# Kernel optimization log

Hardware: AMD Instinct MI355X
Metric: run time of the kernel (lower is better)

The kernel has to match this reference:

```python
import jax, jax.numpy as jnp
import numpy as np

B, N, C, D, H, L, F = 64, 256, 16, 512, 8, 8, 2048
HD = D // H
PI = np.pi


def _ln(x, w, b, eps=1e-5):
    mu = jnp.mean(x, -1, keepdims=True)
    var = jnp.mean(jnp.square(x - mu), -1, keepdims=True)
    return (x - mu) * jax.lax.rsqrt(var + eps) * w + b


def _forward(x_node, x_full, Wp, bp, cls, e_w1, e_b1, e_w2, e_b2, edge_scale,
             qkv_w, qkv_b, out_w, out_b, ln1_w, ln1_b, ln2_w, ln2_b,
             ff1_w, ff1_b, ff2_w, ff2_b, cl_ln_w, cl_ln_b, cl_w1, cl_b1, cl_w2, cl_b2):
    Bq, Nq, _ = x_node.shape
    # pairwise kaon geometry from absolute y/phi
    y = x_full[:, :, 14]
    phi = x_full[:, :, 15]
    dy = jnp.abs(y[:, :, None] - y[:, None, :])                                  # [B,N,N]
    dphi = jnp.abs(jnp.mod(phi[:, :, None] - phi[:, None, :] + PI, 2 * PI) - PI)
    dr = jnp.sqrt(dy * dy + dphi * dphi + 1e-8)
    ef = jnp.stack([dy, dphi, dr], -1)                                           # [B,N,N,3]
    hmid = jax.nn.gelu(ef @ e_w1.T + e_b1, approximate=False)                    # [B,N,N,16]
    raw = hmid @ e_w2.T + e_b2                                                   # [B,N,N,H]
    central = jnp.mean(raw, axis=2).transpose(0, 2, 1)                           # [B,H,N]
    edge_bias = raw.transpose(0, 3, 1, 2)                                        # [B,H,N,N]
    bias = jnp.zeros((Bq, H, Nq + 1, Nq + 1), x_node.dtype)
    bias = bias.at[:, :, 1:, 1:].set(edge_bias)
    bias = bias.at[:, :, 0, 1:].set(central * edge_scale)
    bias = bias.at[:, :, 1:, 0].set(central * edge_scale)

    h = x_node @ Wp.T + bp
    h = jnp.concatenate([jnp.broadcast_to(cls, (Bq, 1, D)), h], axis=1)          # [B,S,D]
    S = Nq + 1
    scale = 1.0 / np.sqrt(HD)
    for l in range(L):  # pre-norm TransformerEncoderLayer (activation=relu, no final norm)
        x = _ln(h, ln1_w[l], ln1_b[l])
        qkv = x @ qkv_w[l].T + qkv_b[l]
        q, k, v = jnp.split(qkv, 3, axis=-1)
        q = q.reshape(Bq, S, H, HD).transpose(0, 2, 1, 3)
        k = k.reshape(Bq, S, H, HD).transpose(0, 2, 1, 3)
        v = v.reshape(Bq, S, H, HD).transpose(0, 2, 1, 3)
        scores = jnp.einsum('bhqd,bhkd->bhqk', q, k) * scale + bias
        attn = jax.nn.softmax(scores, axis=-1)
        o = jnp.einsum('bhqk,bhkd->bhqd', attn, v).transpose(0, 2, 1, 3).reshape(Bq, S, D)
        h = h + o @ out_w[l].T + out_b[l]
        x = _ln(h, ln2_w[l], ln2_b[l])
        h = h + jax.nn.relu(x @ ff1_w[l].T + ff1_b[l]) @ ff2_w[l].T + ff2_b[l]
    x = _ln(h[:, 0], cl_ln_w, cl_ln_b)
    return jax.nn.gelu(x @ cl_w1.T + cl_b1, approximate=False) @ cl_w2.T + cl_b2  # [B,2]


def setup_inputs() -> dict:
    key = jax.random.key(0)
    ks = iter(jax.random.split(key, 40))
    f32 = jnp.float32

    def nrm(shape, s=0.02):
        return (s * jax.random.normal(next(ks), shape)).astype(f32)

    return {
        'x_node': jax.random.normal(next(ks), (B, N, C), f32),
        'x_full': jax.random.normal(next(ks), (B, N, 16), f32),
        'Wp': nrm((D, C)), 'bp': jnp.zeros((D,), f32),
        'cls': nrm((1, 1, D)),
        'e_w1': nrm((16, 3), 0.3), 'e_b1': jnp.zeros((16,), f32),
        'e_w2': nrm((H, 16), 0.01), 'e_b2': jnp.zeros((H,), f32),
        'edge_scale': jnp.full((1,), 0.1, f32),
        'qkv_w': nrm((L, 3 * D, D)), 'qkv_b': jnp.zeros((L, 3 * D), f32),
        'out_w': nrm((L, D, D)), 'out_b': jnp.zeros((L, D), f32),
        'ln1_w': jnp.ones((L, D), f32), 'ln1_b': jnp.zeros((L, D), f32),
        'ln2_w': jnp.ones((L, D), f32), 'ln2_b': jnp.zeros((L, D), f32),
        'ff1_w': nrm((L, F, D)), 'ff1_b': jnp.zeros((L, F), f32),
        'ff2_w': nrm((L, D, F)), 'ff2_b': jnp.zeros((L, D), f32),
        'cl_ln_w': jnp.ones((D,), f32), 'cl_ln_b': jnp.zeros((D,), f32),
        'cl_w1': nrm((D // 2, D)), 'cl_b1': jnp.zeros((D // 2,), f32),
        'cl_w2': nrm((2, D // 2)), 'cl_b2': jnp.zeros((2,), f32),
    }


def reference(x_node, x_full, Wp, bp, cls, e_w1, e_b1, e_w2, e_b2, edge_scale,
              qkv_w, qkv_b, out_w, out_b, ln1_w, ln1_b, ln2_w, ln2_b,
              ff1_w, ff1_b, ff2_w, ff2_b, cl_ln_w, cl_ln_b, cl_w1, cl_b1, cl_w2, cl_b2):
    return _forward(x_node, x_full, Wp, bp, cls, e_w1, e_b1, e_w2, e_b2, edge_scale,
                    qkv_w, qkv_b, out_w, out_b, ln1_w, ln1_b, ln2_w, ln2_b,
                    ff1_w, ff1_b, ff2_w, ff2_b, cl_ln_w, cl_ln_b, cl_w1, cl_b1, cl_w2, cl_b2)
```

## Files before the change

### kernel.cpp

```cpp
#include <hip/hip_runtime.h>
#include <hip/hip_bf16.h>
#include <stdint.h>

#define PI_F     3.14159265358979323846f
#define TWO_PI_F 6.28318530717958647692f

typedef __attribute__((ext_vector_type(8))) short bf16x8;
typedef __attribute__((ext_vector_type(4))) float f32x4;

#define BB 64
#define NN 256
#define SS 257
#define DD 512
#define HH 8
#define HDD 64
#define LL 8
#define MTOK 16448
#define MPAD 16512
#define BSTR 264
#define VSTR 320

__device__ __forceinline__ float b2f(unsigned short u){
  union { float f; uint32_t i; } c; c.i = ((uint32_t)u) << 16; return c.f;
}
__device__ __forceinline__ unsigned short f2b(float f){
  union { float f; uint32_t i; } c; c.f = f;
  uint32_t r = c.i + 0x7FFFu + ((c.i >> 16) & 1u);
  return (unsigned short)(r >> 16);
}

typedef __attribute__((address_space(1))) unsigned char ga_t;
typedef __attribute__((address_space(3))) unsigned char ls_t;
__device__ __forceinline__ void gl_lds16(const void* g, void* l){
  __builtin_amdgcn_global_load_lds((ga_t*)g, (ls_t*)l, 16, 0, 0);
}

__global__ __launch_bounds__(256) void cvt_kernel(const float* __restrict__ src,
                                                  unsigned short* __restrict__ dst, int n2){
  int i = blockIdx.x*256 + threadIdx.x;
  int stride = gridDim.x*256;
  for (; i < n2; i += stride){
    float2 v = ((const float2*)src)[i];
    ((uint32_t*)dst)[i] = (uint32_t)f2b(v.x) | ((uint32_t)f2b(v.y) << 16);
  }
}

__global__ __launch_bounds__(256) void edge_kernel(
    const float* __restrict__ x_full, const float* __restrict__ e_w1, const float* __restrict__ e_b1,
    const float* __restrict__ e_w2, const float* __restrict__ e_b2,
    unsigned short* __restrict__ bias, float* __restrict__ central)
{
  const int bi = blockIdx.x;
  const int b = bi >> 8, i = bi & 255;
  const int j = threadIdx.x;
  const float yi = x_full[((long)b*NN + i)*16 + 14];
  const float fi = x_full[((long)b*NN + i)*16 + 15];
  const float yj = x_full[((long)b*NN + j)*16 + 14];
  const float fj = x_full[((long)b*NN + j)*16 + 15];
  const float dy = fabsf(yi - yj);
  float md = fmodf(fi - fj + PI_F, TWO_PI_F);
  if (md < 0.f) md += TWO_PI_F;
  const float dphi = fabsf(md - PI_F);
  const float dr = sqrtf(dy*dy + dphi*dphi + 1e-8f);
  float raw[8];
  #pragma unroll
  for (int hh = 0; hh < 8; ++hh) raw[hh] = e_b2[hh];
  #pragma unroll
  for (int k = 0; k < 16; ++k){
    float z = e_w1[k*3]*dy + e_w1[k*3+1]*dphi + e_w1[k*3+2]*dr + e_b1[k];
    float g = 0.5f*z*(1.f + erff(z*0.70710678118f));
    #pragma unroll
    for (int hh = 0; hh < 8; ++hh) raw[hh] += g * e_w2[hh*16 + k];
  }
  #pragma unroll
  for (int hh = 0; hh < 8; ++hh)
    bias[(((long)b*HH + hh)*SS + 1 + i)*BSTR + 1 + j] = f2b(raw[hh]);
  #pragma unroll
  for (int m = 1; m < 64; m <<= 1)
    #pragma unroll
    for (int hh = 0; hh < 8; ++hh) raw[hh] += __shfl_xor(raw[hh], m);
  __shared__ float cw[4][8];
  const int wv = j >> 6;
  if ((j & 63) == 0)
    for (int hh = 0; hh < 8; ++hh) cw[wv][hh] = raw[hh];
  __syncthreads();
  if (j < 8){
    float t = cw[0][j] + cw[1][j] + cw[2][j] + cw[3][j];
    central[((long)b*NN + i)*HH + j] = t * (1.f/NN);
  }
}

__global__ __launch_bounds__(256) void edge_border_kernel(
    const float* __restrict__ central, const float* __restrict__ edge_scale,
    unsigned short* __restrict__ bias)
{
  const int bh = blockIdx.x;
  const int b = bh >> 3, h = bh & 7;
  const int j = threadIdx.x;
  const float es = edge_scale[0];
  const float cv = central[((long)b*NN + j)*HH + h] * es;
  const long base = (long)bh*SS*BSTR;
  const unsigned short u = f2b(cv);
  bias[base + 1 + j] = u;
  bias[base + (long)(1+j)*BSTR] = u;
  if (j == 0) bias[base] = 0;
}

__global__ __launch_bounds__(256) void proj_kernel(
    const float* __restrict__ x_node, const float* __restrict__ Wp,
    const float* __restrict__ bp, const float* __restrict__ cls, float* __restrict__ hb)
{
  const int t = blockIdx.x;
  const int tid = threadIdx.x;
  const int b = t / SS, s2 = t - b*SS;
  float2 o;
  if (s2 == 0){
    o = *(const float2*)(cls + tid*2);
  } else {
    const float* xr = x_node + ((long)b*NN + (s2-1))*16;
    float xv[16];
    #pragma unroll
    for (int c2 = 0; c2 < 16; ++c2) xv[c2] = xr[c2];
    float oo[2];
    #pragma unroll
    for (int e = 0; e < 2; ++e){
      int d = tid*2 + e;
      float a = bp[d];
      const float* wr2 = Wp + (long)d*16;
      #pragma unroll
      for (int c2 = 0; c2 < 16; ++c2) a += xv[c2]*wr2[c2];
      oo[e] = a;
    }
    o.x = oo[0]; o.y = oo[1];
  }
  *(float2*)(hb + (long)t*DD + tid*2) = o;
}

__global__ __launch_bounds__(256) void ln_kernel(
    const float* __restrict__ hb, const float* __restrict__ w,
    const float* __restrict__ bbv, unsigned short* __restrict__ xb)
{
  const int t = blockIdx.x;
  const int tid = threadIdx.x;
  const float2 v = *(const float2*)(hb + (long)t*DD + tid*2);
  float s = v.x + v.y;
  float ss = v.x*v.x + v.y*v.y;
  #pragma unroll
  for (int m = 1; m < 64; m <<= 1){ s += __shfl_xor(s, m); ss += __shfl_xor(ss, m); }
  __shared__ float red[8];
  const int wv = tid >> 6;
  if ((tid & 63) == 0){ red[wv] = s; red[4+wv] = ss; }
  __syncthreads();
  s  = red[0]+red[1]+red[2]+red[3];
  ss = red[4]+red[5]+red[6]+red[7];
  const float mu = s * (1.f/DD);
  const float var = ss * (1.f/DD) - mu*mu;
  const float rs = rsqrtf(var + 1e-5f);
  const float2 wv2 = *(const float2*)(w + tid*2);
  const float2 bv2 = *(const float2*)(bbv + tid*2);
  float o0 = (v.x - mu)*rs*wv2.x + bv2.x;
  float o1 = (v.y - mu)*rs*wv2.y + bv2.y;
  ((uint32_t*)xb)[(long)t*256 + tid] = (uint32_t)f2b(o0) | ((uint32_t)f2b(o1) << 16);
}

template<int EPI>
__global__ __launch_bounds__(256, 4) void gemm_kernel(
    const unsigned short* __restrict__ A, const unsigned short* __restrict__ Bw,
    const float* __restrict__ bias, void* __restrict__ Cout,
    int M, int N, int K, int ldc, int nblocks)
{
  __shared__ unsigned short As[128*64];
  __shared__ unsigned short Bs[128*64];
  const int tid = threadIdx.x;
  const int lane = tid & 63;
  const int wave = tid >> 6;
  const int wr = wave >> 1, wc = wave & 1;
  const int l16 = lane & 15, lhi = lane >> 4;

  const int nwg = gridDim.x;
  const int q8 = nwg >> 3, r8 = nwg & 7;
  const int xcd = blockIdx.x & 7, idx = blockIdx.x >> 3;
  const int lin = (xcd < r8 ? xcd*(q8+1) : r8*(q8+1) + (xcd-r8)*q8) + idx;
  const int mb = lin / nblocks;
  const int nb = lin - mb*nblocks;
  const long m0 = (long)mb * 128;
  const long n0 = (long)nb * 128;

  f32x4 acc[4][4];
  const f32x4 z4 = {0.f, 0.f, 0.f, 0.f};
  #pragma unroll
  for (int mi = 0; mi < 4; ++mi)
    #pragma unroll
    for (int ni = 0; ni < 4; ++ni) acc[mi][ni] = z4;

  const char* Ab = (const char*)A;
  const char* Bb = (const char*)Bw;
  const int nkt = K >> 6;
  for (int kt = 0; kt < nkt; ++kt){
    #pragma unroll
    for (int c = 0; c < 4; ++c){
      const int bo = c*4096 + tid*16;
      const int row = bo >> 7;
      const int kb = bo & 127;
      gl_lds16(Ab + ((m0+row)*(long)K)*2 + (long)kt*128 + kb, (char*)As + bo);
      gl_lds16(Bb + ((n0+row)*(long)K)*2 + (long)kt*128 + kb, (char*)Bs + bo);
    }
    __syncthreads();
    #pragma unroll
    for (int kd = 0; kd < 2; ++kd){
      bf16x8 af[4], bfr[4];
      #pragma unroll
      for (int mi = 0; mi < 4; ++mi)
        af[mi] = *(const bf16x8*)((const char*)As + (wr*64 + mi*16 + l16)*128 + kd*64 + lhi*16);
      #pragma unroll
      for (int ni = 0; ni < 4; ++ni)
        bfr[ni] = *(const bf16x8*)((const char*)Bs + (wc*64 + ni*16 + l16)*128 + kd*64 + lhi*16);
      #pragma unroll
      for (int mi = 0; mi < 4; ++mi)
        #pragma unroll
        for (int ni = 0; ni < 4; ++ni)
          acc[mi][ni] = __builtin_amdgcn_mfma_f32_16x16x32_bf16(af[mi], bfr[ni], acc[mi][ni], 0, 0, 0);
    }
    __syncthreads();
  }
  #pragma unroll
  for (int mi = 0; mi < 4; ++mi){
    #pragma unroll
    for (int ni = 0; ni < 4; ++ni){
      const int col = (int)n0 + wc*64 + ni*16 + l16;
      const float bn = bias[col];
      const int rowb = (int)m0 + wr*64 + mi*16 + lhi*4;
      #pragma unroll
      for (int r = 0; r < 4; ++r){
        const int m = rowb + r;
        if (m < M){
          float v = acc[mi][ni][r] + bn;
          if (EPI == 1) v = fmaxf(v, 0.f);
          if (EPI == 2) ((float*)Cout)[(long)m*ldc + col] += v;
          else          ((unsigned short*)Cout)[(long)m*ldc + col] = f2b(v);
        }
      }
    }
  }
}

__global__ __launch_bounds__(256) void vtrans_kernel(
    const unsigned short* __restrict__ qkv, unsigned short* __restrict__ vt)
{
  const int bh = blockIdx.x;
  const int c = blockIdx.y;
  const int b = bh >> 3, h = bh & 7;
  __shared__ unsigned short tile[64][72];
  const int tid = threadIdx.x;
  const int rr = tid >> 3, ch = tid & 7;
  #pragma unroll
  for (int it = 0; it < 2; ++it){
    const int sl = it*32 + rr;
    const long tok = (long)b*SS + c*64 + sl;
    bf16x8 v = *(const bf16x8*)(qkv + tok*1536 + 1024 + h*64 + ch*8);
    *(bf16x8*)(&tile[sl][ch*8]) = v;
  }
  __syncthreads();
  #pragma unroll
  for (int it = 0; it < 2; ++it){
    const int d = it*32 + rr;
    const int s0 = c*64 + ch*8;
    bf16x8 o;
    #pragma unroll
    for (int e = 0; e < 8; ++e){
      const int sgl = s0 + e;
      o[e] = (sgl < SS) ? (short)tile[ch*8 + e][d] : (short)0;
    }
    *(bf16x8*)(vt + ((long)bh*HDD + d)*VSTR + s0) = o;
  }
}

__global__ __launch_bounds__(576) void flash_kernel(
    const unsigned short* __restrict__ qkv, const unsigned short* __restrict__ vt,
    const unsigned short* __restrict__ bias, unsigned short* __restrict__ ob)
{
  const int bh = blockIdx.x;
  const int b = bh >> 3, h = bh & 7;
  const int qt = threadIdx.x >> 6;
  const int lane = threadIdx.x & 63;
  const int l16 = lane & 15, lhi = lane >> 4;

  __shared__ unsigned short Ks[2][2048];
  __shared__ unsigned short Vs[2][2048];
  __shared__ unsigned short Bsh[9][2][1024];
  __shared__ unsigned short pt[9][1024];
  unsigned short* ptw = pt[qt];

  bf16x8 qf[2][2];
  #pragma unroll
  for (int mi = 0; mi < 2; ++mi)
    #pragma unroll
    for (int kd = 0; kd < 2; ++kd){
      const long tok = (long)b*SS + qt*32 + mi*16 + l16;
      qf[mi][kd] = *(const bf16x8*)(qkv + tok*1536 + h*64 + kd*32 + lhi*8);
    }

  auto stage = [&](int jtn, int bb){
    const int rB = lane >> 2, cB = lane & 3;
    const char* gb = (const char*)bias + (((long)bh*SS + qt*32)*BSTR + (long)jtn*32)*2;
    char* lb = (char*)&Bsh[qt][bb][0];
    gl_lds16(gb + (long)rB*BSTR*2        + cB*16, lb + lane*16);
    gl_lds16(gb + (long)(16+rB)*BSTR*2   + cB*16, lb + 1024 + lane*16);
    if (qt < 4){
      const int rK = lane >> 3, cK = lane & 7;
      gl_lds16((const char*)qkv + (((long)b*SS + jtn*32 + qt*8 + rK)*1536 + 512 + h*64)*2 + ((cK ^ rK)*16),
               (char*)&Ks[bb][0] + qt*1024 + lane*16);
    } else if (qt < 8){
      const int rV = lane >> 2, cV = lane & 3;
      const int d = (qt-4)*16 + rV;
      gl_lds16((const char*)vt + (((long)bh*64 + d)*VSTR + (long)jtn*32)*2 + ((cV ^ (rV & 3))*16),
               (char*)&Vs[bb][0] + (qt-4)*1024 + lane*16);
    }
  };

  f32x4 oacc[2][4];
  const f32x4 z4 = {0.f, 0.f, 0.f, 0.f};
  #pragma unroll
  for (int mi = 0; mi < 2; ++mi)
    #pragma unroll
    for (int ni = 0; ni < 4; ++ni) oacc[mi][ni] = z4;
  float mrow[2][4], lrow[2][4];
  #pragma unroll
  for (int mi = 0; mi < 2; ++mi)
    #pragma unroll
    for (int r = 0; r < 4; ++r){ mrow[mi][r] = -1e30f; lrow[mi][r] = 0.f; }

  stage(0, 0);
  __builtin_amdgcn_sched_barrier(0);

  for (int jt = 0; jt < 9; ++jt){
    const int cur = jt & 1;
    if (jt < 8){
      stage(jt+1, cur ^ 1);
      __builtin_amdgcn_sched_barrier(0);
      if (qt < 8) asm volatile("s_waitcnt vmcnt(3)" ::: "memory");
      else        asm volatile("s_waitcnt vmcnt(2)" ::: "memory");
    } else {
      asm volatile("s_waitcnt vmcnt(0)" ::: "memory");
    }
    __builtin_amdgcn_sched_barrier(0);
    __builtin_amdgcn_s_barrier();
    __builtin_amdgcn_sched_barrier(0);

    bf16x8 kf[2][2];
    #pragma unroll
    for (int ni = 0; ni < 2; ++ni)
      #pragma unroll
      for (int kd = 0; kd < 2; ++kd){
        const int row = ni*16 + l16;
        const int sw = (kd*4 + lhi) ^ (row & 7);
        kf[ni][kd] = *(const bf16x8*)((const char*)&Ks[cur][0] + row*128 + sw*16);
      }
    f32x4 sacc[2][2];
    #pragma unroll
    for (int mi = 0; mi < 2; ++mi)
      #pragma unroll
      for (int ni = 0; ni < 2; ++ni) sacc[mi][ni] = z4;
    #pragma unroll
    for (int kd = 0; kd < 2; ++kd)
      #pragma unroll
      for (int mi = 0; mi < 2; ++mi)
        #pragma unroll
        for (int ni = 0; ni < 2; ++ni)
          sacc[mi][ni] = __builtin_amdgcn_mfma_f32_16x16x32_bf16(qf[mi][kd], kf[ni][kd], sacc[mi][ni], 0, 0, 0);

    float sv[2][2][4];
    #pragma unroll
    for (int mi = 0; mi < 2; ++mi)
      #pragma unroll
      for (int ni = 0; ni < 2; ++ni)
        #pragma unroll
        for (int r = 0; r < 4; ++r){
          const int col = jt*32 + ni*16 + l16;
          float x = sacc[mi][ni][r] * 0.125f;
          x += b2f(Bsh[qt][cur][(mi*16 + lhi*4 + r)*32 + ni*16 + l16]);
          if (col >= SS) x = -1e30f;
          sv[mi][ni][r] = x;
        }
    #pragma unroll
    for (int mi = 0; mi < 2; ++mi)
      #pragma unroll
      for (int r = 0; r < 4; ++r){
        float pm = fmaxf(sv[mi][0][r], sv[mi][1][r]);
        #pragma unroll
        for (int sh = 1; sh < 16; sh <<= 1) pm = fmaxf(pm, __shfl_xor(pm, sh));
        const float mold = mrow[mi][r];
        const float mnew = fmaxf(mold, pm);
        const float corr = __expf(mold - mnew);
        mrow[mi][r] = mnew;
        float psum = 0.f;
        #pragma unroll
        for (int ni = 0; ni < 2; ++ni){
          const float p = __expf(sv[mi][ni][r] - mnew);
          sv[mi][ni][r] = p;
          psum += p;
        }
        #pragma unroll
        for (int sh = 1; sh < 16; sh <<= 1) psum += __shfl_xor(psum, sh);
        lrow[mi][r] = lrow[mi][r]*corr + psum;
        #pragma unroll
        for (int ni = 0; ni < 4; ++ni) oacc[mi][ni][r] = oacc[mi][ni][r]*corr;
      }
    #pragma unroll
    for (int mi = 0; mi < 2; ++mi)
      #pragma unroll
      for (int ni = 0; ni < 2; ++ni)
        #pragma unroll
        for (int r = 0; r < 4; ++r)
          ptw[(mi*16 + lhi*4 + r)*32 + ni*16 + l16] = f2b(sv[mi][ni][r]);
    bf16x8 pf[2];
    #pragma unroll
    for (int mi = 0; mi < 2; ++mi)
      pf[mi] = *(const bf16x8*)(ptw + (mi*16 + l16)*32 + lhi*8);
    bf16x8 vf[4];
    #pragma unroll
    for (int ni = 0; ni < 4; ++ni){
      const int d = ni*16 + l16;
      const int sw = lhi ^ (d & 3);
      vf[ni] = *(const bf16x8*)((const char*)&Vs[cur][0] + d*64 + sw*16);
    }
    #pragma unroll
    for (int mi = 0; mi < 2; ++mi)
      #pragma unroll
      for (int ni = 0; ni < 4; ++ni)
        oacc[mi][ni] = __builtin_amdgcn_mfma_f32_16x16x32_bf16(pf[mi], vf[ni], oacc[mi][ni], 0, 0, 0);

    __builtin_amdgcn_sched_barrier(0);
    __builtin_amdgcn_s_barrier();
    __builtin_amdgcn_sched_barrier(0);
  }

  #pragma unroll
  for (int mi = 0; mi < 2; ++mi)
    #pragma unroll
    for (int r = 0; r < 4; ++r){
      const int row = qt*32 + mi*16 + lhi*4 + r;
      if (row < SS){
        const float inv = 1.0f / lrow[mi][r];
        const long tok = (long)b*SS + row;
        #pragma unroll
        for (int ni = 0; ni < 4; ++ni)
          ob[tok*DD + h*HDD + ni*16 + l16] = f2b(oacc[mi][ni][r] * inv);
      }
    }
}

__global__ __launch_bounds__(256) void cls_kernel(
    const float* __restrict__ hb, const float* __restrict__ lw, const float* __restrict__ lb,
    const float* __restrict__ w1, const float* __restrict__ b1,
    const float* __restrict__ w2, const float* __restrict__ b2, float* __restrict__ out)
{
  const int b = blockIdx.x;
  const int tid = threadIdx.x;
  const float* row = hb + (long)b*SS*DD;
  const float2 v = *(const float2*)(row + tid*2);
  float s = v.x + v.y, ss = v.x*v.x + v.y*v.y;
  #pragma unroll
  for (int m = 1; m < 64; m <<= 1){ s += __shfl_xor(s, m); ss += __shfl_xor(ss, m); }
  __shared__ float red[8];
  const int wv = tid >> 6;
  if ((tid & 63) == 0){ red[wv] = s; red[4+wv] = ss; }
  __syncthreads();
  s  = red[0]+red[1]+red[2]+red[3];
  ss = red[4]+red[5]+red[6]+red[7];
  const float mu = s * (1.f/DD);
  const float var = ss * (1.f/DD) - mu*mu;
  const float rs = rsqrtf(var + 1e-5f);
  __shared__ __align__(16) float xs[DD];
  xs[tid*2]   = (v.x - mu)*rs*lw[tid*2]   + lb[tid*2];
  xs[tid*2+1] = (v.y - mu)*rs*lw[tid*2+1] + lb[tid*2+1];
  __syncthreads();
  float a = b1[tid];
  const float4* w1v = (const float4*)(w1 + (long)tid*DD);
  const float4* xsv = (const float4*)xs;
  for (int d4 = 0; d4 < DD/4; ++d4){
    const float4 wv4 = w1v[d4], xv4 = xsv[d4];
    a += wv4.x*xv4.x + wv4.y*xv4.y + wv4.z*xv4.z + wv4.w*xv4.w;
  }
  const float g = 0.5f*a*(1.f + erff(a*0.70710678118f));
  float p0 = g * w2[tid];
  float p1 = g * w2[256 + tid];
  #pragma unroll
  for (int m = 1; m < 64; m <<= 1){ p0 += __shfl_xor(p0, m); p1 += __shfl_xor(p1, m); }
  __shared__ float r2[8];
  if ((tid & 63) == 0){ r2[wv] = p0; r2[4+wv] = p1; }
  __syncthreads();
  if (tid == 0) out[b*2]   = r2[0]+r2[1]+r2[2]+r2[3] + b2[0];
  if (tid == 1) out[b*2+1] = r2[4]+r2[5]+r2[6]+r2[7] + b2[1];
}

extern "C" void kernel_launch(void* const* d_in, const int* in_sizes, int n_in,
                              void* d_out, int out_size, void* d_ws, size_t ws_size,
                              hipStream_t stream) {
  const float* x_node    = (const float*)d_in[0];
  const float* x_full    = (const float*)d_in[1];
  const float* Wp        = (const float*)d_in[2];
  const float* bp        = (const float*)d_in[3];
  const float* cls       = (const float*)d_in[4];
  const float* e_w1      = (const float*)d_in[5];
  const float* e_b1      = (const float*)d_in[6];
  const float* e_w2      = (const float*)d_in[7];
  const float* e_b2      = (const float*)d_in[8];
  const float* edge_scale= (const float*)d_in[9];
  const float* qkv_w     = (const float*)d_in[10];
  const float* qkv_b     = (const float*)d_in[11];
  const float* out_w     = (const float*)d_in[12];
  const float* out_b     = (const float*)d_in[13];
  const float* ln1_w     = (const float*)d_in[14];
  const float* ln1_b     = (const float*)d_in[15];
  const float* ln2_w     = (const float*)d_in[16];
  const float* ln2_b     = (const float*)d_in[17];
  const float* ff1_w     = (const float*)d_in[18];
  const float* ff1_b     = (const float*)d_in[19];
  const float* ff2_w     = (const float*)d_in[20];
  const float* ff2_b     = (const float*)d_in[21];
  const float* cl_ln_w   = (const float*)d_in[22];
  const float* cl_ln_b   = (const float*)d_in[23];
  const float* cl_w1     = (const float*)d_in[24];
  const float* cl_b1     = (const float*)d_in[25];
  const float* cl_w2     = (const float*)d_in[26];
  const float* cl_b2     = (const float*)d_in[27];
  float* out = (float*)d_out;

  char* w = (char*)d_ws;
  size_t off = 0;
  auto take = [&](size_t bytes)->char*{
    char* p = w + off;
    off += (bytes + 255) & ~(size_t)255;
    return p;
  };
  unsigned short* wq8   = (unsigned short*)take((size_t)LL*1536*512*2);
  unsigned short* wo8   = (unsigned short*)take((size_t)LL*512*512*2);
  unsigned short* wf1   = (unsigned short*)take((size_t)LL*2048*512*2);
  unsigned short* wf2   = (unsigned short*)take((size_t)LL*512*2048*2);
  unsigned short* bias16= (unsigned short*)take((size_t)BB*HH*SS*BSTR*2 + 65536);
  float*          cent  = (float*)take((size_t)BB*NN*HH*4);
  float*          hbuf  = (float*)take((size_t)MPAD*DD*4);
  unsigned short* xb    = (unsigned short*)take((size_t)MPAD*DD*2);
  unsigned short* obuf  = (unsigned short*)take((size_t)MPAD*DD*2);
  unsigned short* qkvb  = (unsigned short*)take((size_t)MPAD*1536*2);
  unsigned short* vtb   = (unsigned short*)take((size_t)BB*HH*HDD*VSTR*2);
  unsigned short* ffb   = qkvb;

  cvt_kernel<<<4096, 256, 0, stream>>>(qkv_w, wq8, LL*1536*512/2);
  cvt_kernel<<<4096, 256, 0, stream>>>(out_w, wo8, LL*512*512/2);
  cvt_kernel<<<4096, 256, 0, stream>>>(ff1_w, wf1, LL*2048*512/2);
  cvt_kernel<<<4096, 256, 0, stream>>>(ff2_w, wf2, LL*512*2048/2);

  edge_kernel<<<dim3(BB*NN), 256, 0, stream>>>(x_full, e_w1, e_b1, e_w2, e_b2, bias16, cent);
  edge_border_kernel<<<dim3(BB*HH), 256, 0, stream>>>(cent, edge_scale, bias16);
  proj_kernel<<<dim3(MTOK), 256, 0, stream>>>(x_node, Wp, bp, cls, hbuf);

  for (int l = 0; l < LL; ++l){
    ln_kernel<<<dim3(MTOK), 256, 0, stream>>>(hbuf, ln1_w + l*DD, ln1_b + l*DD, xb);
    gemm_kernel<0><<<dim3(129*12), 256, 0, stream>>>(xb, wq8 + (size_t)l*1536*512,
        qkv_b + (size_t)l*1536, qkvb, MTOK, 1536, 512, 1536, 12);
    vtrans_kernel<<<dim3(512, 5), 256, 0, stream>>>(qkvb, vtb);
    flash_kernel<<<dim3(512), 576, 0, stream>>>(qkvb, vtb, bias16, obuf);
    gemm_kernel<2><<<dim3(129*4), 256, 0, stream>>>(obuf, wo8 + (size_t)l*512*512,
        out_b + (size_t)l*DD, hbuf, MTOK, 512, 512, 512, 4);
    ln_kernel<<<dim3(MTOK), 256, 0, stream>>>(hbuf, ln2_w + l*DD, ln2_b + l*DD, xb);
    gemm_kernel<1><<<dim3(129*16), 256, 0, stream>>>(xb, wf1 + (size_t)l*2048*512,
        ff1_b + (size_t)l*2048, ffb, MTOK, 2048, 512, 2048, 16);
    gemm_kernel<2><<<dim3(129*4), 256, 0, stream>>>(ffb, wf2 + (size_t)l*512*2048,
        ff2_b + (size_t)l*DD, hbuf, MTOK, 512, 2048, 512, 4);
  }
  cls_kernel<<<dim3(BB), 256, 0, stream>>>(hbuf, cl_ln_w, cl_ln_b, cl_w1, cl_b1, cl_w2, cl_b2, out);
}
```

Baseline: 2.775 ms.

## Use one wave per token in layernorm, approximate GELU, add MFMA priority hints

Layernorm now processes four tokens per block, one wave each, with 8-element vector loads and stores, which removes the shared-memory reduction and block barrier. The edge MLP swaps the erf-based GELU for a tanh approximation built on exp, and replaces fmodf with a floor-based wrap. The flash kernel raises wave priority around its MFMA groups. The tanh GELU departs from the exact erf GELU in the reference, so it adds approximation error to the attention bias, though that bias is stored in bf16 anyway.

```diff
diff --git a/kernel.cpp b/kernel.cpp
--- a/kernel.cpp
+++ b/kernel.cpp
@@ -4,6 +4,7 @@
 
 #define PI_F     3.14159265358979323846f
 #define TWO_PI_F 6.28318530717958647692f
+#define INV2PI_F 0.15915494309189535f
 
 typedef __attribute__((ext_vector_type(8))) short bf16x8;
 typedef __attribute__((ext_vector_type(4))) float f32x4;
@@ -28,6 +29,13 @@
   uint32_t r = c.i + 0x7FFFu + ((c.i >> 16) & 1u);
   return (unsigned short)(r >> 16);
 }
+__device__ __forceinline__ float gelu_fast(float z){
+  const float z2 = z*z;
+  const float u2 = z * (1.5957691216f + 0.071354816f*z2);
+  const float e = __expf(u2);
+  const float th = 1.f - 2.f/(1.f + e);
+  return 0.5f*z*(1.f + th);
+}
 
 typedef __attribute__((address_space(1))) unsigned char ga_t;
 typedef __attribute__((address_space(3))) unsigned char ls_t;
@@ -58,8 +66,9 @@
   const float yj = x_full[((long)b*NN + j)*16 + 14];
   const float fj = x_full[((long)b*NN + j)*16 + 15];
   const float dy = fabsf(yi - yj);
-  float md = fmodf(fi - fj + PI_F, TWO_PI_F);
-  if (md < 0.f) md += TWO_PI_F;
+  const float xw = fi - fj + PI_F;
+  const float tw = xw * INV2PI_F;
+  const float md = (tw - floorf(tw)) * TWO_PI_F;
   const float dphi = fabsf(md - PI_F);
   const float dr = sqrtf(dy*dy + dphi*dphi + 1e-8f);
   float raw[8];
@@ -68,7 +77,7 @@
   #pragma unroll
   for (int k = 0; k < 16; ++k){
     float z = e_w1[k*3]*dy + e_w1[k*3+1]*dphi + e_w1[k*3+2]*dr + e_b1[k];
-    float g = 0.5f*z*(1.f + erff(z*0.70710678118f));
+    float g = gelu_fast(z);
     #pragma unroll
     for (int hh = 0; hh < 8; ++hh) raw[hh] += g * e_w2[hh*16 + k];
   }
@@ -140,27 +149,32 @@
     const float* __restrict__ hb, const float* __restrict__ w,
     const float* __restrict__ bbv, unsigned short* __restrict__ xb)
 {
-  const int t = blockIdx.x;
-  const int tid = threadIdx.x;
-  const float2 v = *(const float2*)(hb + (long)t*DD + tid*2);
-  float s = v.x + v.y;
-  float ss = v.x*v.x + v.y*v.y;
+  const int tok = blockIdx.x*4 + (threadIdx.x >> 6);
+  const int lane = threadIdx.x & 63;
+  const float4* p = (const float4*)(hb + (long)tok*DD + lane*8);
+  const float4 a = p[0], bq = p[1];
+  float s  = a.x + a.y + a.z + a.w + bq.x + bq.y + bq.z + bq.w;
+  float ss = a.x*a.x + a.y*a.y + a.z*a.z + a.w*a.w
+           + bq.x*bq.x + bq.y*bq.y + bq.z*bq.z + bq.w*bq.w;
   #pragma unroll
   for (int m = 1; m < 64; m <<= 1){ s += __shfl_xor(s, m); ss += __shfl_xor(ss, m); }
-  __shared__ float red[8];
-  const int wv = tid >> 6;
-  if ((tid & 63) == 0){ red[wv] = s; red[4+wv] = ss; }
-  __syncthreads();
-  s  = red[0]+red[1]+red[2]+red[3];
-  ss = red[4]+red[5]+red[6]+red[7];
   const float mu = s * (1.f/DD);
   const float var = ss * (1.f/DD) - mu*mu;
   const float rs = rsqrtf(var + 1e-5f);
-  const float2 wv2 = *(const float2*)(w + tid*2);
-  const float2 bv2 = *(const float2*)(bbv + tid*2);
-  float o0 = (v.x - mu)*rs*wv2.x + bv2.x;
-  float o1 = (v.y - mu)*rs*wv2.y + bv2.y;
-  ((uint32_t*)xb)[(long)t*256 + tid] = (uint32_t)f2b(o0) | ((uint32_t)f2b(o1) << 16);
+  const float4* wp = (const float4*)(w + lane*8);
+  const float4* bp2 = (const float4*)(bbv + lane*8);
+  const float4 w0 = wp[0], w1 = wp[1];
+  const float4 b0 = bp2[0], b1 = bp2[1];
+  bf16x8 o;
+  o[0] = (short)f2b((a.x - mu)*rs*w0.x + b0.x);
+  o[1] = (short)f2b((a.y - mu)*rs*w0.y + b0.y);
+  o[2] = (short)f2b((a.z - mu)*rs*w0.z + b0.z);
+  o[3] = (short)f2b((a.w - mu)*rs*w0.w + b0.w);
+  o[4] = (short)f2b((bq.x - mu)*rs*w1.x + b1.x);
+  o[5] = (short)f2b((bq.y - mu)*rs*w1.y + b1.y);
+  o[6] = (short)f2b((bq.z - mu)*rs*w1.z + b1.z);
+  o[7] = (short)f2b((bq.w - mu)*rs*w1.w + b1.w);
+  *(bf16x8*)(xb + (long)tok*DD + lane*8) = o;
 }
 
 template<int EPI>
@@ -361,6 +375,7 @@
     for (int mi = 0; mi < 2; ++mi)
       #pragma unroll
       for (int ni = 0; ni < 2; ++ni) sacc[mi][ni] = z4;
+    __builtin_amdgcn_s_setprio(1);
     #pragma unroll
     for (int kd = 0; kd < 2; ++kd)
       #pragma unroll
@@ -368,6 +383,7 @@
         #pragma unroll
         for (int ni = 0; ni < 2; ++ni)
           sacc[mi][ni] = __builtin_amdgcn_mfma_f32_16x16x32_bf16(qf[mi][kd], kf[ni][kd], sacc[mi][ni], 0, 0, 0);
+    __builtin_amdgcn_s_setprio(0);
 
     float sv[2][2][4];
     #pragma unroll
@@ -424,11 +440,13 @@
       const int sw = lhi ^ (d & 3);
       vf[ni] = *(const bf16x8*)((const char*)&Vs[cur][0] + d*64 + sw*16);
     }
+    __builtin_amdgcn_s_setprio(1);
     #pragma unroll
     for (int mi = 0; mi < 2; ++mi)
       #pragma unroll
       for (int ni = 0; ni < 4; ++ni)
         oacc[mi][ni] = __builtin_amdgcn_mfma_f32_16x16x32_bf16(pf[mi], vf[ni], oacc[mi][ni], 0, 0, 0);
+    __builtin_amdgcn_s_setprio(0);
 
     __builtin_amdgcn_sched_barrier(0);
     __builtin_amdgcn_s_barrier();
@@ -557,14 +575,14 @@
   proj_kernel<<<dim3(MTOK), 256, 0, stream>>>(x_node, Wp, bp, cls, hbuf);
 
   for (int l = 0; l < LL; ++l){
-    ln_kernel<<<dim3(MTOK), 256, 0, stream>>>(hbuf, ln1_w + l*DD, ln1_b + l*DD, xb);
+    ln_kernel<<<dim3(MTOK/4), 256, 0, stream>>>(hbuf, ln1_w + l*DD, ln1_b + l*DD, xb);
     gemm_kernel<0><<<dim3(129*12), 256, 0, stream>>>(xb, wq8 + (size_t)l*1536*512,
         qkv_b + (size_t)l*1536, qkvb, MTOK, 1536, 512, 1536, 12);
     vtrans_kernel<<<dim3(512, 5), 256, 0, stream>>>(qkvb, vtb);
     flash_kernel<<<dim3(512), 576, 0, stream>>>(qkvb, vtb, bias16, obuf);
     gemm_kernel<2><<<dim3(129*4), 256, 0, stream>>>(obuf, wo8 + (size_t)l*512*512,
         out_b + (size_t)l*DD, hbuf, MTOK, 512, 512, 512, 4);
-    ln_kernel<<<dim3(MTOK), 256, 0, stream>>>(hbuf, ln2_w + l*DD, ln2_b + l*DD, xb);
+    ln_kernel<<<dim3(MTOK/4), 256, 0, stream>>>(hbuf, ln2_w + l*DD, ln2_b + l*DD, xb);
     gemm_kernel<1><<<dim3(129*16), 256, 0, stream>>>(xb, wf1 + (size_t)l*2048*512,
         ff1_b + (size_t)l*2048, ffb, MTOK, 2048, 512, 2048, 16);
     gemm_kernel<2><<<dim3(129*4), 256, 0, stream>>>(ffb, wf2 + (size_t)l*512*2048,
```

New measurement: 2.675 ms. 3.6% less time.
